# Kernel tuning notes

Measured on AMD Instinct MI355X. Metric: run time of the kernel, lower is better.

Reference implementation:

```python
import jax, jax.numpy as jnp
import numpy as np

# MAML backbone parameter shapes (standard 4-conv few-shot net + 5-way logits head)
PARAM_SHAPES = [(64, 3, 3, 3), (64,), (64, 64, 3, 3), (64,), (64, 64, 3, 3), (64,),
                (64, 64, 3, 3), (64,), (5, 1600), (5,)]
GATE_DIM = 512   # hierarchicalClustering.input_dim + hidden_dim
B = 256          # meta-batch of tasks (vectorized over the original python loop)


def setup_inputs() -> dict:
    key = jax.random.key(0)
    ks = jax.random.split(key, 1 + 3 * len(PARAM_SHAPES))
    inp = {"emb": jax.random.normal(ks[0], (B, GATE_DIM), dtype=jnp.float32)}
    for i, s in enumerate(PARAM_SHAPES):
        n = int(np.prod(s))
        inp[f"p{i}"] = jax.random.normal(ks[1 + 3 * i], s, dtype=jnp.float32) * 0.05
        inp[f"W{i}"] = jax.random.normal(ks[2 + 3 * i], (n, GATE_DIM), dtype=jnp.float32) / np.float32(np.sqrt(GATE_DIM))
        inp[f"b{i}"] = jnp.zeros((n,), dtype=jnp.float32)
    return inp


def reference(emb, p0, W0, b0, p1, W1, b1, p2, W2, b2, p3, W3, b3, p4, W4, b4,
              p5, W5, b5, p6, W6, b6, p7, W7, b7, p8, W8, b8, p9, W9, b9):
    # Per MAML parameter tensor: eta = sigmoid(Linear(emb)); adapted = eta * theta.
    # Loop is over a small fixed set of structurally distinct params (10), vectorized over tasks B.
    triples = [(p0, W0, b0), (p1, W1, b1), (p2, W2, b2), (p3, W3, b3), (p4, W4, b4),
               (p5, W5, b5), (p6, W6, b6), (p7, W7, b7), (p8, W8, b8), (p9, W9, b9)]
    outs = []
    for p, W, b in triples:
        eta = jax.nn.sigmoid(emb @ W.T + b)          # [B, numel_i]
        outs.append(eta * p.reshape(-1))             # adapted theta_i, flattened
    return jnp.concatenate(outs, axis=1)             # [B, total_numel]
```

## Files before the change

kernel.cpp:

```cpp
#include <hip/hip_runtime.h>
#include <hip/hip_bf16.h>

#define GATE 512
#define MROWS 256
#define NTOT 120581
#define CH 16
#define NCH 16

typedef __attribute__((ext_vector_type(8))) short short8;
typedef __attribute__((ext_vector_type(4))) float  f32x4;

struct GemmParams {
    const float* W[10];
    const float* p[10];
    const float* bias[10];
};

__device__ __forceinline__ short bf16bits(float x) {
    __hip_bfloat16 h = __float2bfloat16(x);
    return *reinterpret_cast<short*>(&h);
}

__global__ void emb_to_bf16(const float* __restrict__ emb,
                            unsigned short* __restrict__ o) {
    int i = (blockIdx.x * blockDim.x + threadIdx.x) * 8;
    f32x4 a = *(const f32x4*)(emb + i);
    f32x4 b = *(const f32x4*)(emb + i + 4);
    short8 r;
#pragma unroll
    for (int j = 0; j < 4; ++j) { r[j] = bf16bits(a[j]); r[4 + j] = bf16bits(b[j]); }
    *(short8*)(o + i) = r;
}

__global__ __launch_bounds__(256, 4) void gate_gemm(GemmParams P,
                                                    const unsigned short* __restrict__ embw,
                                                    float* __restrict__ out)
{
    constexpr int kStarts[11] = {0, 1728, 1792, 38656, 38720, 75584,
                                 75648, 112512, 112576, 120576, 120581};
    __shared__ unsigned short Atile[2][CH * GATE];

    const int t    = threadIdx.x;
    const int lane = t & 63;
    const int wave = t >> 6;
    const int lr   = lane & 15;
    const int lg   = lane >> 4;

    const int  n     = blockIdx.x * 64 + wave * 16 + lr;
    const bool valid = n < NTOT;
    const int  nc    = valid ? n : NTOT - 1;
    int tt = 0;
#pragma unroll
    for (int i = 1; i < 10; ++i) tt += (nc >= kStarts[i]);
    const int rr = nc - kStarts[tt];
    const float* wrow = P.W[tt] + (size_t)rr * GATE + lg * 8;
    const float pv = P.p[tt][rr];
    const float bv = P.bias[tt][rr];

    auto stage = [&](int buf, int c) {
#pragma unroll
        for (int i = 0; i < 4; ++i) {
            const int rl = i * 4 + wave;
            const unsigned short* src =
                embw + (size_t)(c * CH + rl) * GATE + ((lane ^ (rl & 7)) * 8);
            unsigned short* dst = &Atile[buf][(size_t)(i * 256 + t) * 8];
            __builtin_amdgcn_global_load_lds(
                (const __attribute__((address_space(1))) void*)src,
                (__attribute__((address_space(3))) void*)dst, 16, 0, 0);
        }
    };

    stage(0, 0);

    short8 Bbf[16];
#pragma unroll
    for (int b = 0; b < 4; ++b) {
        f32x4 raw[8];
#pragma unroll
        for (int j = 0; j < 4; ++j) {
            raw[j * 2 + 0] = *(const f32x4*)(wrow + (b * 4 + j) * 32);
            raw[j * 2 + 1] = *(const f32x4*)(wrow + (b * 4 + j) * 32 + 4);
        }
#pragma unroll
        for (int j = 0; j < 4; ++j) {
            short8 bb;
#pragma unroll
            for (int q = 0; q < 4; ++q) {
                bb[q]     = bf16bits(raw[j * 2][q]);
                bb[4 + q] = bf16bits(raw[j * 2 + 1][q]);
            }
            Bbf[b * 4 + j] = bb;
        }
    }
#pragma unroll
    for (int i = 0; i < 16; ++i)
        asm volatile("" : "+v"(Bbf[i]));

    asm volatile("s_waitcnt vmcnt(0)" ::: "memory");
    __builtin_amdgcn_s_barrier();

#pragma unroll
    for (int c = 0; c < NCH; ++c) {
        const int buf = c & 1;
        if (c + 1 < NCH) stage(buf ^ 1, c + 1);

        f32x4 acc0 = (f32x4){0.f, 0.f, 0.f, 0.f};
        f32x4 acc1 = (f32x4){0.f, 0.f, 0.f, 0.f};
#pragma unroll
        for (int ks = 0; ks < 16; ++ks) {
            const int slot = (ks * 4 + lg) ^ (lr & 7);
            short8 af = *(const short8*)(&Atile[buf][lr * GATE + slot * 8]);
            if (ks & 1) acc1 = __builtin_amdgcn_mfma_f32_16x16x32_bf16(af, Bbf[ks], acc1, 0, 0, 0);
            else        acc0 = __builtin_amdgcn_mfma_f32_16x16x32_bf16(af, Bbf[ks], acc0, 0, 0, 0);
        }

        if (valid) {
            float* ocol = out + n;
            const int m0 = c * CH + lg * 4;
#pragma unroll
            for (int q = 0; q < 4; ++q) {
                float x   = acc0[q] + acc1[q] + bv;
                float e   = __expf(-x);
                float eta = __builtin_amdgcn_rcpf(1.0f + e);
                ocol[(size_t)(m0 + q) * NTOT] = eta * pv;
            }
        }

        if (c + 1 < NCH) {
            asm volatile("s_waitcnt vmcnt(4)" ::: "memory");
            __builtin_amdgcn_s_barrier();
            __builtin_amdgcn_sched_barrier(0);
        }
    }
}

extern "C" void kernel_launch(void* const* d_in, const int* in_sizes, int n_in,
                              void* d_out, int out_size, void* d_ws, size_t ws_size,
                              hipStream_t stream) {
    const float* emb = (const float*)d_in[0];
    GemmParams P;
    for (int i = 0; i < 10; ++i) {
        P.p[i]    = (const float*)d_in[1 + 3 * i];
        P.W[i]    = (const float*)d_in[2 + 3 * i];
        P.bias[i] = (const float*)d_in[3 + 3 * i];
    }

    unsigned short* embw = (unsigned short*)d_ws;
    emb_to_bf16<<<(MROWS * GATE) / (256 * 8), 256, 0, stream>>>(emb, embw);

    int nblocks = (NTOT + 63) / 64;
    gate_gemm<<<nblocks, 256, 0, stream>>>(P, embw, (float*)d_out);
}
```

Before: 118.1 us.

## Triple-buffer the embedding tile in LDS with two-chunk prefetch distance

The LDS staging buffer for the bf16 embedding chunk grows from two to three slots, and the prefetch now runs two chunks ahead instead of one, so global-to-LDS loads have more time to land before they are consumed. The vmcnt waits are recomputed so they account for the output stores that are in flight between stages, with a separate count for waves whose columns are entirely past the end. The weight-row load loop is reordered to issue four vector loads per step without changing which data lands where. In exchange, LDS per block rises to 48KB and the launch-bounds occupancy hint drops from 4 to 3 blocks per CU, which may reduce latency hiding for a kernel dominated by output writes.

Result: no change. 118.0 us (-0.2%).

```diff
diff --git a/kernel.cpp b/kernel.cpp
--- a/kernel.cpp
+++ b/kernel.cpp
@@ -32,13 +32,13 @@
     *(short8*)(o + i) = r;
 }
 
-__global__ __launch_bounds__(256, 4) void gate_gemm(GemmParams P,
+__global__ __launch_bounds__(256, 3) void gate_gemm(GemmParams P,
                                                     const unsigned short* __restrict__ embw,
                                                     float* __restrict__ out)
 {
     constexpr int kStarts[11] = {0, 1728, 1792, 38656, 38720, 75584,
                                  75648, 112512, 112576, 120576, 120581};
-    __shared__ unsigned short Atile[2][CH * GATE];
+    __shared__ unsigned short Atile[3][CH * GATE];
 
     const int t    = threadIdx.x;
     const int lane = t & 63;
@@ -46,8 +46,9 @@
     const int lr   = lane & 15;
     const int lg   = lane >> 4;
 
-    const int  n     = blockIdx.x * 64 + wave * 16 + lr;
-    const bool valid = n < NTOT;
+    const int  n       = blockIdx.x * 64 + wave * 16 + lr;
+    const bool valid   = n < NTOT;
+    const bool wstores = (blockIdx.x * 64 + wave * 16) < NTOT;
     const int  nc    = valid ? n : NTOT - 1;
     int tt = 0;
 #pragma unroll
@@ -71,26 +72,23 @@
     };
 
     stage(0, 0);
+    stage(1, 1);
 
     short8 Bbf[16];
 #pragma unroll
-    for (int b = 0; b < 4; ++b) {
-        f32x4 raw[8];
+    for (int b = 0; b < 8; ++b) {
+        f32x4 r0 = *(const f32x4*)(wrow + b * 64);
+        f32x4 r1 = *(const f32x4*)(wrow + b * 64 + 4);
+        f32x4 r2 = *(const f32x4*)(wrow + b * 64 + 32);
+        f32x4 r3 = *(const f32x4*)(wrow + b * 64 + 36);
+        short8 b0, b1;
 #pragma unroll
-        for (int j = 0; j < 4; ++j) {
-            raw[j * 2 + 0] = *(const f32x4*)(wrow + (b * 4 + j) * 32);
-            raw[j * 2 + 1] = *(const f32x4*)(wrow + (b * 4 + j) * 32 + 4);
+        for (int q = 0; q < 4; ++q) {
+            b0[q] = bf16bits(r0[q]); b0[4 + q] = bf16bits(r1[q]);
+            b1[q] = bf16bits(r2[q]); b1[4 + q] = bf16bits(r3[q]);
         }
-#pragma unroll
-        for (int j = 0; j < 4; ++j) {
-            short8 bb;
-#pragma unroll
-            for (int q = 0; q < 4; ++q) {
-                bb[q]     = bf16bits(raw[j * 2][q]);
-                bb[4 + q] = bf16bits(raw[j * 2 + 1][q]);
-            }
-            Bbf[b * 4 + j] = bb;
-        }
+        Bbf[2 * b]     = b0;
+        Bbf[2 * b + 1] = b1;
     }
 #pragma unroll
     for (int i = 0; i < 16; ++i)
@@ -101,8 +99,8 @@
 
 #pragma unroll
     for (int c = 0; c < NCH; ++c) {
-        const int buf = c & 1;
-        if (c + 1 < NCH) stage(buf ^ 1, c + 1);
+        const int buf = c % 3;
+        if (c + 2 < NCH) stage((c + 2) % 3, c + 2);
 
         f32x4 acc0 = (f32x4){0.f, 0.f, 0.f, 0.f};
         f32x4 acc1 = (f32x4){0.f, 0.f, 0.f, 0.f};
@@ -127,7 +125,12 @@
         }
 
         if (c + 1 < NCH) {
-            asm volatile("s_waitcnt vmcnt(4)" ::: "memory");
+            if (c < NCH - 2) {
+                if (wstores) asm volatile("s_waitcnt vmcnt(12)" ::: "memory");
+                else         asm volatile("s_waitcnt vmcnt(4)"  ::: "memory");
+            } else {
+                asm volatile("s_waitcnt vmcnt(0)" ::: "memory");
+            }
             __builtin_amdgcn_s_barrier();
             __builtin_amdgcn_sched_barrier(0);
         }
```

## Make gate GEMM persistent with resident half-emb tile and prefetched weight panels

Applied to the files above, without the earlier changes.

Replaces the one-block-per-64-columns grid with 512 persistent blocks of 512 threads. Each block loads half of the bf16 embedding rows (128x512) into LDS once and then strides over 128-column weight panels. While MFMAs run on the current panel, the next panel's weights are loaded and converted to bf16 into a second register set. The aim is to stop restreaming the embedding per block and to hide weight-load latency. In exchange it uses more LDS and registers per block, which lowers occupancy, and every weight row is now read by two blocks.

Result: slower. 249.4 us (+111.1%).

```diff
diff --git a/kernel.cpp b/kernel.cpp
--- a/kernel.cpp
+++ b/kernel.cpp
@@ -2,10 +2,9 @@
 #include <hip/hip_bf16.h>
 
 #define GATE 512
-#define MROWS 256
 #define NTOT 120581
-#define CH 16
-#define NCH 16
+#define NPAN 943
+#define HALF 128
 
 typedef __attribute__((ext_vector_type(8))) short short8;
 typedef __attribute__((ext_vector_type(4))) float  f32x4;
@@ -32,13 +31,13 @@
     *(short8*)(o + i) = r;
 }
 
-__global__ __launch_bounds__(256, 4) void gate_gemm(GemmParams P,
+__global__ __launch_bounds__(512, 2) void gate_gemm(GemmParams P,
                                                     const unsigned short* __restrict__ embw,
                                                     float* __restrict__ out)
 {
     constexpr int kStarts[11] = {0, 1728, 1792, 38656, 38720, 75584,
                                  75648, 112512, 112576, 120576, 120581};
-    __shared__ unsigned short Atile[2][CH * GATE];
+    __shared__ unsigned short Atile[HALF * GATE];
 
     const int t    = threadIdx.x;
     const int lane = t & 63;
@@ -46,91 +45,134 @@
     const int lr   = lane & 15;
     const int lg   = lane >> 4;
 
-    const int  n     = blockIdx.x * 64 + wave * 16 + lr;
-    const bool valid = n < NTOT;
-    const int  nc    = valid ? n : NTOT - 1;
-    int tt = 0;
+    const int half = blockIdx.x & 1;
+    const int p0   = blockIdx.x >> 1;
+
 #pragma unroll
-    for (int i = 1; i < 10; ++i) tt += (nc >= kStarts[i]);
-    const int rr = nc - kStarts[tt];
-    const float* wrow = P.W[tt] + (size_t)rr * GATE + lg * 8;
-    const float pv = P.p[tt][rr];
-    const float bv = P.bias[tt][rr];
+    for (int i = 0; i < 16; ++i) {
+        const int rl = wave * 16 + i;
+        const unsigned short* src =
+            embw + (size_t)(half * HALF + rl) * GATE + ((lane ^ (rl & 7)) * 8);
+        unsigned short* dst = &Atile[rl * GATE + lane * 8];
+        __builtin_amdgcn_global_load_lds(
+            (const __attribute__((address_space(1))) void*)src,
+            (__attribute__((address_space(3))) void*)dst, 16, 0, 0);
+    }
 
-    auto stage = [&](int buf, int c) {
+    auto colmeta = [&](int pan, const float*& wr, float& pv, float& bv,
+                       int& n, bool& valid) {
+        n = pan * 128 + wave * 16 + lr;
+        valid = n < NTOT;
+        int nc = valid ? n : NTOT - 1;
+        int tt = 0;
 #pragma unroll
-        for (int i = 0; i < 4; ++i) {
-            const int rl = i * 4 + wave;
-            const unsigned short* src =
-                embw + (size_t)(c * CH + rl) * GATE + ((lane ^ (rl & 7)) * 8);
-            unsigned short* dst = &Atile[buf][(size_t)(i * 256 + t) * 8];
-            __builtin_amdgcn_global_load_lds(
-                (const __attribute__((address_space(1))) void*)src,
-                (__attribute__((address_space(3))) void*)dst, 16, 0, 0);
-        }
+        for (int i = 1; i < 10; ++i) tt += (nc >= kStarts[i]);
+        int rr = nc - kStarts[tt];
+        wr = P.W[tt] + (size_t)rr * GATE + lg * 8;
+        pv = P.p[tt][rr];
+        bv = P.bias[tt][rr];
     };
 
-    stage(0, 0);
-
-    short8 Bbf[16];
+    short8 B0[16], B1[16];
+    {
+        const float* wr; float pv, bv; int n; bool v;
+        colmeta(p0, wr, pv, bv, n, v);
 #pragma unroll
-    for (int b = 0; b < 4; ++b) {
-        f32x4 raw[8];
+        for (int b = 0; b < 8; ++b) {
+            f32x4 r0 = *(const f32x4*)(wr + b * 64);
+            f32x4 r1 = *(const f32x4*)(wr + b * 64 + 4);
+            f32x4 r2 = *(const f32x4*)(wr + b * 64 + 32);
+            f32x4 r3 = *(const f32x4*)(wr + b * 64 + 36);
+            short8 x0, x1;
 #pragma unroll
-        for (int j = 0; j < 4; ++j) {
-            raw[j * 2 + 0] = *(const f32x4*)(wrow + (b * 4 + j) * 32);
-            raw[j * 2 + 1] = *(const f32x4*)(wrow + (b * 4 + j) * 32 + 4);
+            for (int q = 0; q < 4; ++q) {
+                x0[q] = bf16bits(r0[q]); x0[4 + q] = bf16bits(r1[q]);
+                x1[q] = bf16bits(r2[q]); x1[4 + q] = bf16bits(r3[q]);
+            }
+            B0[2 * b] = x0; B0[2 * b + 1] = x1;
         }
 #pragma unroll
-        for (int j = 0; j < 4; ++j) {
-            short8 bb;
-#pragma unroll
-            for (int q = 0; q < 4; ++q) {
-                bb[q]     = bf16bits(raw[j * 2][q]);
-                bb[4 + q] = bf16bits(raw[j * 2 + 1][q]);
-            }
-            Bbf[b * 4 + j] = bb;
-        }
+        for (int i = 0; i < 16; ++i) asm volatile("" : "+v"(B0[i]));
     }
-#pragma unroll
-    for (int i = 0; i < 16; ++i)
-        asm volatile("" : "+v"(Bbf[i]));
 
     asm volatile("s_waitcnt vmcnt(0)" ::: "memory");
     __builtin_amdgcn_s_barrier();
 
+    auto body = [&](short8 (&Bcur)[16], short8 (&Bnext)[16], int pan, int pnext) {
+        const float* wrc; float pv, bv; int n; bool valid;
+        colmeta(pan, wrc, pv, bv, n, valid);
+        const float* wrn; float pvn, bvn; int nn; bool vn;
+        colmeta(pnext, wrn, pvn, bvn, nn, vn);
+        float* ocol = out + n;
+
+        f32x4 rawA[4], rawB[4];
 #pragma unroll
-    for (int c = 0; c < NCH; ++c) {
-        const int buf = c & 1;
-        if (c + 1 < NCH) stage(buf ^ 1, c + 1);
+        for (int ch = 0; ch < 8; ++ch) {
+            {
+                f32x4* raw = (ch & 1) ? rawB : rawA;
+                raw[0] = *(const f32x4*)(wrn + ch * 64);
+                raw[1] = *(const f32x4*)(wrn + ch * 64 + 4);
+                raw[2] = *(const f32x4*)(wrn + ch * 64 + 32);
+                raw[3] = *(const f32x4*)(wrn + ch * 64 + 36);
+            }
 
-        f32x4 acc0 = (f32x4){0.f, 0.f, 0.f, 0.f};
-        f32x4 acc1 = (f32x4){0.f, 0.f, 0.f, 0.f};
+            f32x4 acc0 = (f32x4){0.f, 0.f, 0.f, 0.f};
+            f32x4 acc1 = (f32x4){0.f, 0.f, 0.f, 0.f};
 #pragma unroll
-        for (int ks = 0; ks < 16; ++ks) {
-            const int slot = (ks * 4 + lg) ^ (lr & 7);
-            short8 af = *(const short8*)(&Atile[buf][lr * GATE + slot * 8]);
-            if (ks & 1) acc1 = __builtin_amdgcn_mfma_f32_16x16x32_bf16(af, Bbf[ks], acc1, 0, 0, 0);
-            else        acc0 = __builtin_amdgcn_mfma_f32_16x16x32_bf16(af, Bbf[ks], acc0, 0, 0, 0);
+            for (int ks = 0; ks < 16; ++ks) {
+                const int slot = (ks * 4 + lg) ^ (lr & 7);
+                short8 af = *(const short8*)(&Atile[(ch * 16 + lr) * GATE + slot * 8]);
+                if (ks & 1) acc1 = __builtin_amdgcn_mfma_f32_16x16x32_bf16(af, Bcur[ks], acc1, 0, 0, 0);
+                else        acc0 = __builtin_amdgcn_mfma_f32_16x16x32_bf16(af, Bcur[ks], acc0, 0, 0, 0);
+            }
+
+            if (ch > 0) {
+                f32x4* rp = (ch & 1) ? rawA : rawB;
+                short8 x0, x1;
+#pragma unroll
+                for (int q = 0; q < 4; ++q) {
+                    x0[q] = bf16bits(rp[0][q]); x0[4 + q] = bf16bits(rp[1][q]);
+                    x1[q] = bf16bits(rp[2][q]); x1[4 + q] = bf16bits(rp[3][q]);
+                }
+                Bnext[2 * (ch - 1)]     = x0;
+                Bnext[2 * (ch - 1) + 1] = x1;
+                asm volatile("" : "+v"(Bnext[2 * (ch - 1)]), "+v"(Bnext[2 * (ch - 1) + 1]));
+            }
+
+            if (valid) {
+                const int m0 = half * HALF + ch * 16 + lg * 4;
+#pragma unroll
+                for (int q = 0; q < 4; ++q) {
+                    float x   = acc0[q] + acc1[q] + bv;
+                    float e   = __expf(-x);
+                    float eta = __builtin_amdgcn_rcpf(1.0f + e);
+                    ocol[(size_t)(m0 + q) * NTOT] = eta * pv;
+                }
+            }
         }
-
-        if (valid) {
-            float* ocol = out + n;
-            const int m0 = c * CH + lg * 4;
+        {
+            short8 x0, x1;
 #pragma unroll
             for (int q = 0; q < 4; ++q) {
-                float x   = acc0[q] + acc1[q] + bv;
-                float e   = __expf(-x);
-                float eta = __builtin_amdgcn_rcpf(1.0f + e);
-                ocol[(size_t)(m0 + q) * NTOT] = eta * pv;
+                x0[q] = bf16bits(rawB[0][q]); x0[4 + q] = bf16bits(rawB[1][q]);
+                x1[q] = bf16bits(rawB[2][q]); x1[4 + q] = bf16bits(rawB[3][q]);
             }
+            Bnext[14] = x0; Bnext[15] = x1;
+            asm volatile("" : "+v"(Bnext[14]), "+v"(Bnext[15]));
         }
+    };
 
-        if (c + 1 < NCH) {
-            asm volatile("s_waitcnt vmcnt(4)" ::: "memory");
-            __builtin_amdgcn_s_barrier();
-            __builtin_amdgcn_sched_barrier(0);
-        }
+    int  pan  = p0;
+    bool flip = false;
+    while (true) {
+        const int  pn   = pan + 256;
+        const bool last = pn >= NPAN;
+        const int  pnc  = last ? pan : pn;
+        if (!flip) body(B0, B1, pan, pnc);
+        else       body(B1, B0, pan, pnc);
+        if (last) break;
+        pan  = pn;
+        flip = !flip;
     }
 }
 
@@ -146,8 +188,7 @@
     }
 
     unsigned short* embw = (unsigned short*)d_ws;
-    emb_to_bf16<<<(MROWS * GATE) / (256 * 8), 256, 0, stream>>>(emb, embw);
+    emb_to_bf16<<<(256 * GATE) / (256 * 8), 256, 0, stream>>>(emb, embw);
 
-    int nblocks = (NTOT + 63) / 64;
-    gate_gemm<<<nblocks, 256, 0, stream>>>(P, embw, (float*)d_out);
+    gate_gemm<<<512, 512, 0, stream>>>(P, embw, (float*)d_out);
 }
```
